# Kernel tuning notes

Hardware: AMD Instinct MI355X
Metric: run time of the kernel (lower is better)

The kernel has to match this reference:

```python
import jax, jax.numpy as jnp
import numpy as np

B, C, H = 32, 1000, 512
N = C + 1  # graph nodes = 1 query node + C class nodes
ALPHA_IT = 0.7
BETA_IT = 0.5


def setup_inputs() -> dict:
    key = jax.random.key(0)
    ks = jax.random.split(key, 6)
    stdv = 1.0 / np.sqrt(H)
    return {
        "input_text": jax.random.normal(ks[0], (B, 1, H), jnp.float32),
        "input_img": jax.random.normal(ks[1], (B, 1, H), jnp.float32),
        "base_text_features": jax.random.normal(ks[2], (B, C, H), jnp.float32),
        "base_img_features": jax.random.normal(ks[3], (B, C, H), jnp.float32),
        "W_tt": jax.random.uniform(ks[4], (H, H), jnp.float32, -stdv, stdv),
        "b_tt": jnp.zeros((N, H), jnp.float32),
        "W_it": jax.random.uniform(ks[5], (H, H), jnp.float32, -stdv, stdv),
        "b_it": jnp.zeros((N, H), jnp.float32),
    }


def _cosine_adj(feat):
    # feat: [B, H, N]; F.normalize over dim=1 (feature axis), then x^T x -> [B, N, N]
    xn = feat / jnp.maximum(jnp.linalg.norm(feat, axis=1, keepdims=True), 1e-12)
    return jnp.einsum('bhn,bhm->bnm', xn, xn)


def _gcn(feat, adj, W, b):
    # feat: [B, H, N], adj: [B, N, N]
    adj = jnp.clip(adj, 0.0, None) + jnp.eye(adj.shape[1], dtype=adj.dtype)[None]
    # symmetric norm D^-1/2 A D^-1/2 as a row/col rescale (math-equivalent to diag bmm)
    d = jax.lax.rsqrt(adj.sum(-1))  # [B, N]
    adj = d[:, :, None] * adj * d[:, None, :]
    pre_sup = jnp.einsum('bhn,hk->bnk', feat, W)           # x.T @ W
    out = jnp.einsum('bnm,bmk->bnk', adj, pre_sup) + b[None]
    return jnp.tanh(out[:, 0, :])  # take node 0, apply Tanh -> [B, H]


def reference(input_text, input_img, base_text_features, base_img_features,
              W_tt, b_tt, W_it, b_it):
    # feats built under no_grad + detach in the original
    feat_tt = jax.lax.stop_gradient(
        jnp.concatenate([input_text, base_text_features], axis=1).transpose(0, 2, 1))  # [B,H,N]
    feat_it = jax.lax.stop_gradient(
        jnp.concatenate([input_img, base_img_features], axis=1).transpose(0, 2, 1))
    edge_tt = jax.lax.stop_gradient(_cosine_adj(feat_tt))
    edge_it = jax.lax.stop_gradient(_cosine_adj(feat_it))

    g_tt = _gcn(feat_tt, edge_tt, W_tt, b_tt)  # [B, H]
    g_it = _gcn(feat_it, edge_it, W_it, b_it)
    graph_o = (ALPHA_IT * g_tt + (1.0 - ALPHA_IT) * g_it)[:, None, :]  # [B,1,H]

    out_text = BETA_IT * base_text_features + (1.0 - BETA_IT) * graph_o
    out_img = BETA_IT * base_img_features + (1.0 - BETA_IT) * graph_o
    return (out_text, out_img)
```

## Files before the change

### kernel.cpp

```cpp
#include <hip/hip_runtime.h>
#include <hip/hip_bf16.h>

#define B_ 32
#define C_ 1000
#define H_ 512
#define NP 1024

typedef __attribute__((ext_vector_type(4))) int i32x4;

__device__ __forceinline__ float tanh_fast(float x) {
  float ax = fminf(fabsf(x), 15.0f);
  float e = __expf(2.0f * ax);
  float t = (e - 1.0f) / (e + 1.0f);
  return copysignf(t, x);
}
__device__ __forceinline__ void gload16(const void* g, void* l) {
  __builtin_amdgcn_global_load_lds((const __attribute__((address_space(1))) unsigned*)g,
                                   (__attribute__((address_space(3))) unsigned*)l, 16, 0, 0);
}
__device__ __forceinline__ float sc2f(unsigned v) {
  return (float)(int)(signed char)v;
}

__global__ __launch_bounds__(256) void k_norm(const float* __restrict__ it, const float* __restrict__ ii,
                                              const float* __restrict__ bt, const float* __restrict__ bi,
                                              signed char* __restrict__ xq, float* __restrict__ nrm,
                                              float* __restrict__ qs, float* __restrict__ zero_base) {
  int zi = blockIdx.x * 256 + threadIdx.x;
  if (zi < 114688) zero_base[zi] = 0.0f;

  int wid = blockIdx.x * 4 + (threadIdx.x >> 6);
  int lane = threadIdx.x & 63;
  int node = wid & (NP - 1);
  int mb = wid >> 10;
  int b = mb & 31, mod = mb >> 5;
  const float* src = nullptr;
  if (node == 0) src = (mod ? ii : it) + b * H_;
  else if (node <= C_) src = (mod ? bi : bt) + ((size_t)b * C_ + (node - 1)) * H_;
  float4 v0 = make_float4(0.f, 0.f, 0.f, 0.f), v1 = v0;
  if (src) {
    const float4* s4 = (const float4*)src;
    v0 = s4[lane * 2]; v1 = s4[lane * 2 + 1];
  }
  float ss = v0.x*v0.x + v0.y*v0.y + v0.z*v0.z + v0.w*v0.w
           + v1.x*v1.x + v1.y*v1.y + v1.z*v1.z + v1.w*v1.w;
  #pragma unroll
  for (int o = 32; o; o >>= 1) ss += __shfl_xor(ss, o);
  float n = sqrtf(ss);
  if (lane == 0) nrm[wid] = n;
  float inv = 1.0f / fmaxf(n, 1e-12f);
  float x[8] = {v0.x*inv, v0.y*inv, v0.z*inv, v0.w*inv, v1.x*inv, v1.y*inv, v1.z*inv, v1.w*inv};
  float m8 = 0.f;
  #pragma unroll
  for (int j = 0; j < 8; ++j) m8 = fmaxf(m8, fabsf(x[j]));
  #pragma unroll
  for (int o = 32; o; o >>= 1) m8 = fmaxf(m8, __shfl_xor(m8, o));
  if (lane == 0) qs[wid] = m8 * (1.0f / 127.0f);
  float invq = (m8 > 0.f) ? 127.0f / m8 : 0.f;
  int q[8];
  #pragma unroll
  for (int j = 0; j < 8; ++j) q[j] = __float2int_rn(x[j] * invq);
  unsigned lo = (q[0] & 255) | ((q[1] & 255) << 8) | ((q[2] & 255) << 16) | ((unsigned)(q[3] & 255) << 24);
  unsigned hi = (q[4] & 255) | ((q[5] & 255) << 8) | ((q[6] & 255) << 16) | ((unsigned)(q[7] & 255) << 24);
  *(uint2*)(xq + (size_t)wid * H_ + lane * 8) = make_uint2(lo, hi);
}

__global__ __launch_bounds__(256) void k_gram(const signed char* __restrict__ xq,
                                              const float* __restrict__ qs,
                                              float* __restrict__ r, float* __restrict__ sc) {
  __shared__ __align__(16) unsigned char As[2 * 128 * 64];
  __shared__ __align__(16) unsigned char Bs[2 * 128 * 64];
  __shared__ float s_qs[256];
  int orig = blockIdx.x;
  int xcd = orig & 7;
  int k = orig >> 3;
  int mb = xcd + 8 * (k / 36);
  int idx = k % 36;
  int ti = 0, rem = idx;
  while (rem >= 8 - ti) { rem -= 8 - ti; ++ti; }
  int tj = ti + rem;
  bool diag = (ti == tj);
  const signed char* X = xq + (size_t)mb * NP * H_;
  int tid = threadIdx.x;
  int w = tid >> 6, lane = tid & 63;
  int wr = w >> 1, wc = w & 1;

  if (tid < 128) s_qs[tid] = qs[mb * NP + ti * 128 + tid];
  else           s_qs[tid] = qs[mb * NP + tj * 128 + (tid - 128)];

  i32x4 acc[4][4] = {};
  int lrow = lane >> 2;
  int ps0 = lane & 3;

  auto stage = [&](int buf, int ks) {
    #pragma unroll
    for (int q = 0; q < 2; ++q) {
      int chunk = w * 2 + q;
      int row = chunk * 16 + lrow;
      int qq = ps0 ^ ((row >> 1) & 3);
      gload16(X + (size_t)(ti * 128 + row) * H_ + ks * 64 + qq * 16,
              (void*)(As + buf * 8192 + chunk * 1024));
      if (!diag)
        gload16(X + (size_t)(tj * 128 + row) * H_ + ks * 64 + qq * 16,
                (void*)(Bs + buf * 8192 + chunk * 1024));
    }
  };

  stage(0, 0);
  int cur = 0;
  for (int ks = 0; ks < 8; ++ks) {
    __syncthreads();
    if (ks < 7) stage(cur ^ 1, ks + 1);
    const unsigned char* Ab = As + cur * 8192;
    const unsigned char* Bb = (diag ? As : Bs) + cur * 8192;
    i32x4 af[4], bf[4];
    #pragma unroll
    for (int mi = 0; mi < 4; ++mi) {
      int row = wr * 64 + mi * 16 + (lane & 15);
      int ps = (lane >> 4) ^ ((row >> 1) & 3);
      af[mi] = *(const i32x4*)(Ab + row * 64 + ps * 16);
    }
    #pragma unroll
    for (int ni = 0; ni < 4; ++ni) {
      int row = wc * 64 + ni * 16 + (lane & 15);
      int ps = (lane >> 4) ^ ((row >> 1) & 3);
      bf[ni] = *(const i32x4*)(Bb + row * 64 + ps * 16);
    }
    #pragma unroll
    for (int mi = 0; mi < 4; ++mi)
      #pragma unroll
      for (int ni = 0; ni < 4; ++ni)
        acc[mi][ni] = __builtin_amdgcn_mfma_i32_16x16x64_i8(af[mi], bf[ni], acc[mi][ni], 0, 0, 0);
    cur ^= 1;
  }

  float* rr = r + mb * NP;
  float qsc[4];
  #pragma unroll
  for (int ni = 0; ni < 4; ++ni) qsc[ni] = s_qs[128 + wc * 64 + ni * 16 + (lane & 15)];
  #pragma unroll
  for (int mi = 0; mi < 4; ++mi) {
    #pragma unroll
    for (int reg = 0; reg < 4; ++reg) {
      float v = 0.f;
      #pragma unroll
      for (int ni = 0; ni < 4; ++ni) {
        int d = acc[mi][ni][reg];
        v += (d > 0 ? (float)d : 0.f) * qsc[ni];
      }
      v += __shfl_xor(v, 1); v += __shfl_xor(v, 2); v += __shfl_xor(v, 4); v += __shfl_xor(v, 8);
      if ((lane & 15) == 0) {
        int rloc = wr * 64 + mi * 16 + (lane >> 4) * 4 + reg;
        atomicAdd(&rr[ti * 128 + rloc], v * s_qs[rloc]);
      }
    }
  }
  if (!diag) {
    #pragma unroll
    for (int ni = 0; ni < 4; ++ni) {
      float s = 0.f;
      #pragma unroll
      for (int mi = 0; mi < 4; ++mi)
        #pragma unroll
        for (int reg = 0; reg < 4; ++reg) {
          int d = acc[mi][ni][reg];
          s += (d > 0 ? (float)d : 0.f) * s_qs[wr * 64 + mi * 16 + (lane >> 4) * 4 + reg];
        }
      s += __shfl_xor(s, 16); s += __shfl_xor(s, 32);
      if (lane < 16) {
        int cloc = wc * 64 + ni * 16 + lane;
        atomicAdd(&rr[tj * 128 + cloc], s * s_qs[128 + cloc]);
      }
    }
  }
  if (ti == 0 && wr == 0 && (lane >> 4) == 0) {
    float q0 = s_qs[0];
    float* scc = sc + mb * NP;
    #pragma unroll
    for (int ni = 0; ni < 4; ++ni) {
      int col = tj * 128 + wc * 64 + ni * 16 + (lane & 15);
      int d = acc[0][ni][0];
      scc[col] = (d > 0 ? (float)d : 0.f) * q0 * qsc[ni];
    }
  }
}

__global__ __launch_bounds__(256) void k_y(const signed char* __restrict__ xq,
                                           const float* __restrict__ r, const float* __restrict__ sc,
                                           const float* __restrict__ nrm, const float* __restrict__ qs,
                                           float* __restrict__ y) {
  __shared__ float s_w[128];
  __shared__ __align__(16) float s_part[4][512];
  int bid = blockIdx.x;
  int chunk = bid & 7, mb = bid >> 3;
  int m0 = chunk * 128;
  int t = threadIdx.x;
  const float* rr = r + mb * NP;
  if (t < 128) {
    int m = m0 + t;
    float wm = 0.f;
    if (m < 1001) {
      float d0 = rsqrtf(rr[0] + 1.0f);
      float dm = rsqrtf(rr[m] + 1.0f);
      wm = d0 * dm * (sc[mb * NP + m] + (m == 0 ? 1.0f : 0.0f)) * nrm[mb * NP + m] * qs[mb * NP + m];
    }
    s_w[t] = wm;
  }
  __syncthreads();
  int w = t >> 6, lane = t & 63;
  float a[8] = {};
  const signed char* X = xq + (size_t)mb * NP * H_ + lane * 8;
  for (int i = 0; i < 32; ++i) {
    int m = w * 32 + i;
    float wm = s_w[m];
    uint2 v = *(const uint2*)(X + (size_t)(m0 + m) * H_);
    a[0] = fmaf(wm, sc2f(v.x), a[0]);
    a[1] = fmaf(wm, sc2f(v.x >> 8), a[1]);
    a[2] = fmaf(wm, sc2f(v.x >> 16), a[2]);
    a[3] = fmaf(wm, sc2f(v.x >> 24), a[3]);
    a[4] = fmaf(wm, sc2f(v.y), a[4]);
    a[5] = fmaf(wm, sc2f(v.y >> 8), a[5]);
    a[6] = fmaf(wm, sc2f(v.y >> 16), a[6]);
    a[7] = fmaf(wm, sc2f(v.y >> 24), a[7]);
  }
  #pragma unroll
  for (int j = 0; j < 4; ++j) s_part[w][lane * 8 + j] = a[j];
  #pragma unroll
  for (int j = 4; j < 8; ++j) s_part[w][lane * 8 + j] = a[j];
  __syncthreads();
  float v0 = s_part[0][t] + s_part[1][t] + s_part[2][t] + s_part[3][t];
  float v1 = s_part[0][t + 256] + s_part[1][t + 256] + s_part[2][t + 256] + s_part[3][t + 256];
  atomicAdd(&y[mb * H_ + t], v0);
  atomicAdd(&y[mb * H_ + t + 256], v1);
}

__global__ __launch_bounds__(256) void k_go(const float* __restrict__ y,
                                            const float* __restrict__ Wtt, const float* __restrict__ btt,
                                            const float* __restrict__ Wit, const float* __restrict__ bit,
                                            float* __restrict__ go) {
  int mb = blockIdx.x;
  int b = mb & 31, mod = mb >> 5;
  const float* W = mod ? Wit : Wtt;
  const float* bias = mod ? bit : btt;
  float coef = mod ? 0.3f : 0.7f;
  const float* yy = y + mb * H_;
  int t = threadIdx.x;
  #pragma unroll
  for (int k = t; k < H_; k += 256) {
    float a = bias[k];
    for (int h = 0; h < H_; ++h) a = fmaf(yy[h], W[h * H_ + k], a);
    atomicAdd(&go[b * H_ + k], coef * tanh_fast(a));
  }
}

__global__ __launch_bounds__(256) void k_out(const signed char* __restrict__ xq,
                                             const float* __restrict__ nrm, const float* __restrict__ qs,
                                             const float* __restrict__ go, float* __restrict__ out) {
  int wid = blockIdx.x * 4 + (threadIdx.x >> 6);
  int lane = threadIdx.x & 63;
  int mod = wid >= 32000 ? 1 : 0;
  int rrow = wid - mod * 32000;
  int b = rrow / 1000;
  int c = rrow - b * 1000;
  int mb = mod * 32 + b;
  size_t node_off = (size_t)(mb * NP + c + 1);
  float hnq = 0.5f * nrm[node_off] * qs[node_off];
  uint2 x = *(const uint2*)(xq + node_off * H_ + lane * 8);
  const float4* g4 = (const float4*)(go + b * H_ + lane * 8);
  float4 g0 = g4[0], g1 = g4[1];
  float4 o0, o1;
  o0.x = fmaf(hnq, sc2f(x.x), 0.5f * g0.x);
  o0.y = fmaf(hnq, sc2f(x.x >> 8), 0.5f * g0.y);
  o0.z = fmaf(hnq, sc2f(x.x >> 16), 0.5f * g0.z);
  o0.w = fmaf(hnq, sc2f(x.x >> 24), 0.5f * g0.w);
  o1.x = fmaf(hnq, sc2f(x.y), 0.5f * g1.x);
  o1.y = fmaf(hnq, sc2f(x.y >> 8), 0.5f * g1.y);
  o1.z = fmaf(hnq, sc2f(x.y >> 16), 0.5f * g1.z);
  o1.w = fmaf(hnq, sc2f(x.y >> 24), 0.5f * g1.w);
  float4* o4 = (float4*)(out + (size_t)wid * H_ + lane * 8);
  o4[0] = o0; o4[1] = o1;
}

extern "C" void kernel_launch(void* const* d_in, const int* in_sizes, int n_in,
                              void* d_out, int out_size, void* d_ws, size_t ws_size,
                              hipStream_t stream) {
  const float* it  = (const float*)d_in[0];
  const float* ii  = (const float*)d_in[1];
  const float* bt  = (const float*)d_in[2];
  const float* bi  = (const float*)d_in[3];
  const float* Wtt = (const float*)d_in[4];
  const float* btt = (const float*)d_in[5];
  const float* Wit = (const float*)d_in[6];
  const float* bit = (const float*)d_in[7];

  char* ws = (char*)d_ws;
  signed char* xq = (signed char*)ws;
  size_t off = 33554432;
  float* nrm = (float*)(ws + off); off += 262144;
  float* qs  = (float*)(ws + off); off += 262144;
  float* sc  = (float*)(ws + off); off += 262144;
  float* r   = (float*)(ws + off); off += 262144;
  float* y   = (float*)(ws + off); off += 131072;
  float* go  = (float*)(ws + off); off += 65536;

  k_norm<<<16384, 256, 0, stream>>>(it, ii, bt, bi, xq, nrm, qs, r );
  k_gram<<<64 * 36, 256, 0, stream>>>(xq, qs, r, sc);
  k_y<<<512, 256, 0, stream>>>(xq, r, sc, nrm, qs, y);
  k_go<<<64, 256, 0, stream>>>(y, Wtt, btt, Wit, bit, go);
  k_out<<<16000, 256, 0, stream>>>(xq, nrm, qs, go, (float*)d_out);
}
```

Before: 143.6 us.

## Load Gram MFMA operands directly from global memory and split k_go across more blocks

The int8 Gram kernel no longer stages tiles into shared memory through a double-buffered global_load_lds pipeline. Each lane now reads its MFMA fragments straight from global memory (L2-resident) with a fully unrolled K loop. This removes the per-step barriers and LDS traffic, but gives up explicit prefetch overlap and the diagonal-tile reuse of the A buffer. Separately, k_go launches twice as many blocks, each computing one output column per thread with an unrolled inner loop, to raise parallelism in that small GEMV.

```diff
diff --git a/kernel.cpp b/kernel.cpp
--- a/kernel.cpp
+++ b/kernel.cpp
@@ -13,10 +13,6 @@
   float e = __expf(2.0f * ax);
   float t = (e - 1.0f) / (e + 1.0f);
   return copysignf(t, x);
-}
-__device__ __forceinline__ void gload16(const void* g, void* l) {
-  __builtin_amdgcn_global_load_lds((const __attribute__((address_space(1))) unsigned*)g,
-                                   (__attribute__((address_space(3))) unsigned*)l, 16, 0, 0);
 }
 __device__ __forceinline__ float sc2f(unsigned v) {
   return (float)(int)(signed char)v;
@@ -68,8 +64,6 @@
 __global__ __launch_bounds__(256) void k_gram(const signed char* __restrict__ xq,
                                               const float* __restrict__ qs,
                                               float* __restrict__ r, float* __restrict__ sc) {
-  __shared__ __align__(16) unsigned char As[2 * 128 * 64];
-  __shared__ __align__(16) unsigned char Bs[2 * 128 * 64];
   __shared__ float s_qs[256];
   int orig = blockIdx.x;
   int xcd = orig & 7;
@@ -88,52 +82,25 @@
   if (tid < 128) s_qs[tid] = qs[mb * NP + ti * 128 + tid];
   else           s_qs[tid] = qs[mb * NP + tj * 128 + (tid - 128)];
 
+  const signed char* Ab = X + (size_t)(ti * 128 + wr * 64 + (lane & 15)) * H_ + (lane >> 4) * 16;
+  const signed char* Bb = X + (size_t)(tj * 128 + wc * 64 + (lane & 15)) * H_ + (lane >> 4) * 16;
+
   i32x4 acc[4][4] = {};
-  int lrow = lane >> 2;
-  int ps0 = lane & 3;
-
-  auto stage = [&](int buf, int ks) {
-    #pragma unroll
-    for (int q = 0; q < 2; ++q) {
-      int chunk = w * 2 + q;
-      int row = chunk * 16 + lrow;
-      int qq = ps0 ^ ((row >> 1) & 3);
-      gload16(X + (size_t)(ti * 128 + row) * H_ + ks * 64 + qq * 16,
-              (void*)(As + buf * 8192 + chunk * 1024));
-      if (!diag)
-        gload16(X + (size_t)(tj * 128 + row) * H_ + ks * 64 + qq * 16,
-                (void*)(Bs + buf * 8192 + chunk * 1024));
-    }
-  };
-
-  stage(0, 0);
-  int cur = 0;
+  #pragma unroll
   for (int ks = 0; ks < 8; ++ks) {
-    __syncthreads();
-    if (ks < 7) stage(cur ^ 1, ks + 1);
-    const unsigned char* Ab = As + cur * 8192;
-    const unsigned char* Bb = (diag ? As : Bs) + cur * 8192;
     i32x4 af[4], bf[4];
     #pragma unroll
-    for (int mi = 0; mi < 4; ++mi) {
-      int row = wr * 64 + mi * 16 + (lane & 15);
-      int ps = (lane >> 4) ^ ((row >> 1) & 3);
-      af[mi] = *(const i32x4*)(Ab + row * 64 + ps * 16);
-    }
-    #pragma unroll
-    for (int ni = 0; ni < 4; ++ni) {
-      int row = wc * 64 + ni * 16 + (lane & 15);
-      int ps = (lane >> 4) ^ ((row >> 1) & 3);
-      bf[ni] = *(const i32x4*)(Bb + row * 64 + ps * 16);
-    }
+    for (int mi = 0; mi < 4; ++mi) af[mi] = *(const i32x4*)(Ab + (size_t)mi * 16 * H_ + ks * 64);
+    #pragma unroll
+    for (int ni = 0; ni < 4; ++ni) bf[ni] = *(const i32x4*)(Bb + (size_t)ni * 16 * H_ + ks * 64);
     #pragma unroll
     for (int mi = 0; mi < 4; ++mi)
       #pragma unroll
       for (int ni = 0; ni < 4; ++ni)
         acc[mi][ni] = __builtin_amdgcn_mfma_i32_16x16x64_i8(af[mi], bf[ni], acc[mi][ni], 0, 0, 0);
-    cur ^= 1;
-  }
-
+  }
+
+  __syncthreads();
   float* rr = r + mb * NP;
   float qsc[4];
   #pragma unroll
@@ -224,9 +191,7 @@
     a[7] = fmaf(wm, sc2f(v.y >> 24), a[7]);
   }
   #pragma unroll
-  for (int j = 0; j < 4; ++j) s_part[w][lane * 8 + j] = a[j];
-  #pragma unroll
-  for (int j = 4; j < 8; ++j) s_part[w][lane * 8 + j] = a[j];
+  for (int j = 0; j < 8; ++j) s_part[w][lane * 8 + j] = a[j];
   __syncthreads();
   float v0 = s_part[0][t] + s_part[1][t] + s_part[2][t] + s_part[3][t];
   float v1 = s_part[0][t + 256] + s_part[1][t + 256] + s_part[2][t + 256] + s_part[3][t + 256];
@@ -238,19 +203,18 @@
                                             const float* __restrict__ Wtt, const float* __restrict__ btt,
                                             const float* __restrict__ Wit, const float* __restrict__ bit,
                                             float* __restrict__ go) {
-  int mb = blockIdx.x;
+  int bid = blockIdx.x;
+  int mb = bid & 63, half = bid >> 6;
   int b = mb & 31, mod = mb >> 5;
   const float* W = mod ? Wit : Wtt;
   const float* bias = mod ? bit : btt;
   float coef = mod ? 0.3f : 0.7f;
   const float* yy = y + mb * H_;
-  int t = threadIdx.x;
-  #pragma unroll
-  for (int k = t; k < H_; k += 256) {
-    float a = bias[k];
-    for (int h = 0; h < H_; ++h) a = fmaf(yy[h], W[h * H_ + k], a);
-    atomicAdd(&go[b * H_ + k], coef * tanh_fast(a));
-  }
+  int k = half * 256 + threadIdx.x;
+  float a = bias[k];
+  #pragma unroll 8
+  for (int h = 0; h < H_; ++h) a = fmaf(yy[h], W[h * H_ + k], a);
+  atomicAdd(&go[b * H_ + k], coef * tanh_fast(a));
 }
 
 __global__ __launch_bounds__(256) void k_out(const signed char* __restrict__ xq,
@@ -306,6 +270,6 @@
   k_norm<<<16384, 256, 0, stream>>>(it, ii, bt, bi, xq, nrm, qs, r );
   k_gram<<<64 * 36, 256, 0, stream>>>(xq, qs, r, sc);
   k_y<<<512, 256, 0, stream>>>(xq, r, sc, nrm, qs, y);
-  k_go<<<64, 256, 0, stream>>>(y, Wtt, btt, Wit, bit, go);
+  k_go<<<128, 256, 0, stream>>>(y, Wtt, btt, Wit, bit, go);
   k_out<<<16000, 256, 0, stream>>>(xq, nrm, qs, go, (float*)d_out);
 }
```

Measured after the change: 170.9 us. 1.19x slower.
